# Optimization experiments

Measured on AMD Instinct MI355X. Metric: run time of the kernel, lower is better.

Reference implementation:

```python
import jax, jax.numpy as jnp
import numpy as np

EMBED_DIM = 1024
NUM_HEADS = 16
HEAD_DIM = EMBED_DIM // NUM_HEADS  # 64
SCALE = HEAD_DIM ** -0.5


def _rope_table(seq_len, dtype=jnp.float32):
    # inv_freq: [head_dim/2]
    inv_freq = 1.0 / (10000.0 ** (jnp.arange(0, HEAD_DIM, 2, dtype=dtype) / HEAD_DIM))
    t = jnp.arange(seq_len, dtype=dtype)
    freqs = t[:, None] * inv_freq[None, :]  # [S, hd/2]
    return jnp.sin(freqs), jnp.cos(freqs)


def _apply_rope(x, sin, cos):
    # x: [B, H, S, hd]; sin/cos: [S, hd/2]
    sin = sin[None, None]
    cos = cos[None, None]
    x_even = x[..., 0::2]
    x_odd = x[..., 1::2]
    new_even = x_even * cos - x_odd * sin
    new_odd = x_even * sin + x_odd * cos
    # interleave back: [..., hd/2, 2] -> [..., hd]
    return jnp.stack((new_even, new_odd), axis=-1).reshape(x.shape)


def setup_inputs() -> dict:
    key = jax.random.key(0)
    ks = jax.random.split(key, 9)
    B, S, D = 2, 2048, EMBED_DIM
    s = D ** -0.5
    return {
        "query": jax.random.normal(ks[0], (B, S, D), dtype=jnp.float32),
        "Wq": jax.random.normal(ks[1], (2 * D, D), dtype=jnp.float32) * s,
        "bq": jnp.zeros((2 * D,), dtype=jnp.float32),
        "Wk": jax.random.normal(ks[2], (D, D), dtype=jnp.float32) * s,
        "bk": jnp.zeros((D,), dtype=jnp.float32),
        "Wv": jax.random.normal(ks[3], (D, D), dtype=jnp.float32) * s,
        "bv": jnp.zeros((D,), dtype=jnp.float32),
        "Wo": jax.random.normal(ks[4], (D, D), dtype=jnp.float32) * s,
        "bo": jnp.zeros((D,), dtype=jnp.float32),
    }


def reference(query, Wq, bq, Wk, bk, Wv, bv, Wo, bo):
    B, S, D = query.shape
    H, hd = NUM_HEADS, HEAD_DIM

    # QKV projections (elementwise-gate variant: q_proj outputs 2*D)
    q_raw = (query @ Wq.T + bq).reshape(B, S, H, 2 * hd)
    q = q_raw[..., :hd].transpose(0, 2, 1, 3)          # [B,H,S,hd]
    gate = q_raw[..., hd:].transpose(0, 2, 1, 3)        # [B,H,S,hd]
    k = (query @ Wk.T + bk).reshape(B, S, H, hd).transpose(0, 2, 1, 3)
    v = (query @ Wv.T + bv).reshape(B, S, H, hd).transpose(0, 2, 1, 3)

    sin, cos = _rope_table(S)
    q = _apply_rope(q, sin, cos)
    k = _apply_rope(k, sin, cos)

    # scaled dot-product attention (no mask, non-causal, dropout=0)
    scores = jnp.einsum('bhqd,bhkd->bhqk', q, k) * SCALE
    probs = jax.nn.softmax(scores, axis=-1)
    attn = jnp.einsum('bhqk,bhkd->bhqd', probs, v)

    # sigmoid elementwise gate, then output projection
    attn = attn * jax.nn.sigmoid(gate)
    out = attn.transpose(0, 2, 1, 3).reshape(B, S, D)
    return out @ Wo.T + bo
```

## Files before the change

### kernel.cpp

```cpp
#include <hip/hip_runtime.h>
#include <math.h>

#define SEQ 2048
#define DIMD 1024
#define NH 16
#define HDIM 64

typedef _Float16 h8 __attribute__((ext_vector_type(8)));
typedef _Float16 h4 __attribute__((ext_vector_type(4)));
typedef __fp16 fp16x2 __attribute__((ext_vector_type(2)));
typedef float f32x4 __attribute__((ext_vector_type(4)));

__device__ __forceinline__ int SWE(int r, int c) {
  return ((r << 6) + c) ^ ((r & 7) << 3);
}

#define R0 16384
#define R1 (R0 + 1048576)
#define R2 (R1 + 524288)
#define R3 (R2 + 262144)
#define R4 (R3 + 262144)
#define R5 (R4 + 262144)

__global__ void prep_kernel(const float* __restrict__ query,
                            const float* __restrict__ Wq,
                            const float* __restrict__ Wk,
                            const float* __restrict__ Wv,
                            const float* __restrict__ Wo,
                            _Float16* __restrict__ Ah,
                            _Float16* __restrict__ Wqh,
                            _Float16* __restrict__ Wkh,
                            _Float16* __restrict__ Wvh,
                            _Float16* __restrict__ Woh,
                            _Float16* __restrict__ Wol,
                            float* __restrict__ sintab,
                            float* __restrict__ costab) {
  int i = blockIdx.x * 256 + threadIdx.x;
  if (i < R0) {
#pragma unroll
    for (int j = 0; j < 4; ++j) {
      int idx = i * 4 + j;
      int tp = idx >> 5;
      int fi = idx & 31;
      double inv = pow(10000.0, -(double)(2 * fi) / 64.0);
      double a = (double)tp * inv;
      sintab[idx] = (float)sin(a);
      costab[idx] = (float)cos(a);
    }
    return;
  }
  const float* src;
  _Float16* dst;
  int k;
  if (i < R1) {
    k = i - R0; src = query; dst = Ah;
  } else if (i < R2) {
    k = i - R1; src = Wq; dst = Wqh;
  } else if (i < R3) {
    k = i - R2; src = Wk; dst = Wkh;
  } else if (i < R4) {
    k = i - R3; src = Wv; dst = Wvh;
  } else if (i < R5) {
    k = i - R4;
    float4 v = ((const float4*)Wo)[k];
    h4 H, L;
    H[0] = (_Float16)v.x; L[0] = (_Float16)(v.x - (float)H[0]);
    H[1] = (_Float16)v.y; L[1] = (_Float16)(v.y - (float)H[1]);
    H[2] = (_Float16)v.z; L[2] = (_Float16)(v.z - (float)H[2]);
    H[3] = (_Float16)v.w; L[3] = (_Float16)(v.w - (float)H[3]);
    ((h4*)Woh)[k] = H;
    ((h4*)Wol)[k] = L;
    return;
  } else {
    return;
  }
  float4 v = ((const float4*)src)[k];
  h4 H;
  H[0] = (_Float16)v.x;
  H[1] = (_Float16)v.y;
  H[2] = (_Float16)v.z;
  H[3] = (_Float16)v.w;
  ((h4*)dst)[k] = H;
}

__global__ __launch_bounds__(256, 3) void qkv_kernel(
    const _Float16* __restrict__ Ah, const _Float16* __restrict__ Wqh,
    const _Float16* __restrict__ Wkh, const _Float16* __restrict__ Wvh,
    const float* __restrict__ bq, const float* __restrict__ bk,
    const float* __restrict__ bv, _Float16* __restrict__ qw,
    _Float16* __restrict__ sg, _Float16* __restrict__ kw,
    _Float16* __restrict__ vtw, const float* __restrict__ sintab,
    const float* __restrict__ costab) {
  __shared__ _Float16 Ash[8192];
  __shared__ _Float16 Bsh[8192];
  const int t = threadIdx.x;
  const int lane = t & 63;
  const int w = t >> 6;
  const int wm = w & 1, wn = w >> 1;
  const int fr = lane & 15;
  const int g = lane >> 4;
  const int m0 = blockIdx.y * 128;
  const int n0 = blockIdx.x * 128;
  const int region = (n0 < 2048) ? 0 : (n0 < 3072 ? 1 : 2);
  const _Float16* Wb = region == 0   ? Wqh + (size_t)n0 * DIMD
                       : region == 1 ? Wkh + (size_t)(n0 - 2048) * DIMD
                                     : Wvh + (size_t)(n0 - 3072) * DIMD;
  const float* bias = region == 0   ? bq + n0
                      : region == 1 ? bk + (n0 - 2048)
                                    : bv + (n0 - 3072);

  f32x4 acc[4][4];
#pragma unroll
  for (int i = 0; i < 4; ++i)
#pragma unroll
    for (int j = 0; j < 4; ++j) acc[i][j] = (f32x4){0.f, 0.f, 0.f, 0.f};

  const int srow = t >> 1;
  const int sc = (t & 1) * 32;
  const _Float16* pA = Ah + (size_t)(m0 + srow) * DIMD + sc;
  const _Float16* pW = Wb + (size_t)srow * DIMD + sc;

  h8 ra0 = *(const h8*)(pA);
  h8 ra1 = *(const h8*)(pA + 8);
  h8 ra2 = *(const h8*)(pA + 16);
  h8 ra3 = *(const h8*)(pA + 24);
  h8 rb0 = *(const h8*)(pW);
  h8 rb1 = *(const h8*)(pW + 8);
  h8 rb2 = *(const h8*)(pW + 16);
  h8 rb3 = *(const h8*)(pW + 24);

  for (int k0 = 0; k0 < DIMD; k0 += 64) {
    __syncthreads();
    *(h8*)&Ash[SWE(srow, sc + 0)] = ra0;
    *(h8*)&Ash[SWE(srow, sc + 8)] = ra1;
    *(h8*)&Ash[SWE(srow, sc + 16)] = ra2;
    *(h8*)&Ash[SWE(srow, sc + 24)] = ra3;
    *(h8*)&Bsh[SWE(srow, sc + 0)] = rb0;
    *(h8*)&Bsh[SWE(srow, sc + 8)] = rb1;
    *(h8*)&Bsh[SWE(srow, sc + 16)] = rb2;
    *(h8*)&Bsh[SWE(srow, sc + 24)] = rb3;
    __syncthreads();
    if (k0 + 64 < DIMD) {
      ra0 = *(const h8*)(pA + k0 + 64);
      ra1 = *(const h8*)(pA + k0 + 72);
      ra2 = *(const h8*)(pA + k0 + 80);
      ra3 = *(const h8*)(pA + k0 + 88);
      rb0 = *(const h8*)(pW + k0 + 64);
      rb1 = *(const h8*)(pW + k0 + 72);
      rb2 = *(const h8*)(pW + k0 + 80);
      rb3 = *(const h8*)(pW + k0 + 88);
    }
#pragma unroll
    for (int s = 0; s < 2; ++s) {
      h8 av[4], bv[4];
#pragma unroll
      for (int mi = 0; mi < 4; ++mi)
        av[mi] = *(const h8*)&Ash[SWE(wm * 64 + mi * 16 + fr, 8 * g + 32 * s)];
#pragma unroll
      for (int ni = 0; ni < 4; ++ni)
        bv[ni] = *(const h8*)&Bsh[SWE(wn * 64 + ni * 16 + fr, 8 * g + 32 * s)];
      __builtin_amdgcn_s_setprio(1);
#pragma unroll
      for (int mi = 0; mi < 4; ++mi)
#pragma unroll
        for (int ni = 0; ni < 4; ++ni)
          acc[mi][ni] = __builtin_amdgcn_mfma_f32_16x16x32_f16(
              av[mi], bv[ni], acc[mi][ni], 0, 0, 0);
      __builtin_amdgcn_s_setprio(0);
    }
  }

#pragma unroll
  for (int mi = 0; mi < 4; ++mi)
#pragma unroll
    for (int ni = 0; ni < 4; ++ni) {
      const int cl = wn * 64 + ni * 16 + fr;
      const float bsv = bias[cl];
#pragma unroll
      for (int r = 0; r < 4; ++r) {
        const int row = m0 + wm * 64 + mi * 16 + (lane >> 4) * 4 + r;
        float v = acc[mi][ni][r] + bsv;
        const int b = row >> 11;
        const int s = row & (SEQ - 1);
        if (region == 0) {
          const int h = n0 >> 7;
          const int d = cl & 63;
          if (wn == 0) {
            float vp = __shfl_xor(v, 1);
            const int pi = s * 32 + (d >> 1);
            float sn = sintab[pi], cs = costab[pi];
            float rv = (d & 1) ? (vp * sn + v * cs) : (v * cs - vp * sn);
            rv *= 0.125f;
            qw[((size_t)(b * NH + h) * SEQ + s) * HDIM + d] = (_Float16)rv;
          } else {
            float gv = 1.0f / (1.0f + __expf(-v));
            sg[((size_t)(b * SEQ + s)) * DIMD + h * HDIM + d] = (_Float16)gv;
          }
        } else if (region == 1) {
          const int kc = (n0 - 2048) + cl;
          const int h = kc >> 6, d = kc & 63;
          float vp = __shfl_xor(v, 1);
          const int pi = s * 32 + (d >> 1);
          float sn = sintab[pi], cs = costab[pi];
          float rv = (d & 1) ? (vp * sn + v * cs) : (v * cs - vp * sn);
          kw[((size_t)(b * NH + h) * SEQ + s) * HDIM + d] = (_Float16)rv;
        } else {
          const int vc = (n0 - 3072) + cl;
          const int h = vc >> 6, d = vc & 63;
          vtw[((size_t)(b * NH + h) * HDIM + d) * SEQ + s] = (_Float16)v;
        }
      }
    }
}

__global__ __launch_bounds__(256, 2) void ogemm_kernel(
    const _Float16* __restrict__ Ah, const _Float16* __restrict__ Al,
    const _Float16* __restrict__ Wh, const _Float16* __restrict__ Wl,
    const float* __restrict__ bias, float* __restrict__ out) {
  __shared__ _Float16 Ash[8192];
  __shared__ _Float16 Asl[8192];
  __shared__ _Float16 Bsh[4096];
  __shared__ _Float16 Bsl[4096];
  const int t = threadIdx.x;
  const int lane = t & 63;
  const int w = t >> 6;
  const int wm = w & 1, wn = w >> 1;
  const int fr = lane & 15;
  const int g = lane >> 4;
  const int m0 = blockIdx.y * 128, n0 = blockIdx.x * 64;

  f32x4 acc[4][2];
#pragma unroll
  for (int i = 0; i < 4; ++i)
#pragma unroll
    for (int j = 0; j < 2; ++j) acc[i][j] = (f32x4){0.f, 0.f, 0.f, 0.f};

  const int arow = t >> 1;
  const int ac = (t & 1) * 32;
  const int brow = t >> 2;
  const int bc = (t & 3) * 16;
  const _Float16* pAh = Ah + (size_t)(m0 + arow) * DIMD + ac;
  const _Float16* pAl = Al + (size_t)(m0 + arow) * DIMD + ac;
  const _Float16* pWh = Wh + (size_t)(n0 + brow) * DIMD + bc;
  const _Float16* pWl = Wl + (size_t)(n0 + brow) * DIMD + bc;

  h8 rah0 = *(const h8*)(pAh);
  h8 rah1 = *(const h8*)(pAh + 8);
  h8 rah2 = *(const h8*)(pAh + 16);
  h8 rah3 = *(const h8*)(pAh + 24);
  h8 ral0 = *(const h8*)(pAl);
  h8 ral1 = *(const h8*)(pAl + 8);
  h8 ral2 = *(const h8*)(pAl + 16);
  h8 ral3 = *(const h8*)(pAl + 24);
  h8 rbh0 = *(const h8*)(pWh);
  h8 rbh1 = *(const h8*)(pWh + 8);
  h8 rbl0 = *(const h8*)(pWl);
  h8 rbl1 = *(const h8*)(pWl + 8);

  for (int k0 = 0; k0 < DIMD; k0 += 64) {
    __syncthreads();
    *(h8*)&Ash[SWE(arow, ac + 0)] = rah0;
    *(h8*)&Ash[SWE(arow, ac + 8)] = rah1;
    *(h8*)&Ash[SWE(arow, ac + 16)] = rah2;
    *(h8*)&Ash[SWE(arow, ac + 24)] = rah3;
    *(h8*)&Asl[SWE(arow, ac + 0)] = ral0;
    *(h8*)&Asl[SWE(arow, ac + 8)] = ral1;
    *(h8*)&Asl[SWE(arow, ac + 16)] = ral2;
    *(h8*)&Asl[SWE(arow, ac + 24)] = ral3;
    *(h8*)&Bsh[SWE(brow, bc + 0)] = rbh0;
    *(h8*)&Bsh[SWE(brow, bc + 8)] = rbh1;
    *(h8*)&Bsl[SWE(brow, bc + 0)] = rbl0;
    *(h8*)&Bsl[SWE(brow, bc + 8)] = rbl1;
    __syncthreads();
    if (k0 + 64 < DIMD) {
      rah0 = *(const h8*)(pAh + k0 + 64);
      rah1 = *(const h8*)(pAh + k0 + 72);
      rah2 = *(const h8*)(pAh + k0 + 80);
      rah3 = *(const h8*)(pAh + k0 + 88);
      ral0 = *(const h8*)(pAl + k0 + 64);
      ral1 = *(const h8*)(pAl + k0 + 72);
      ral2 = *(const h8*)(pAl + k0 + 80);
      ral3 = *(const h8*)(pAl + k0 + 88);
      rbh0 = *(const h8*)(pWh + k0 + 64);
      rbh1 = *(const h8*)(pWh + k0 + 72);
      rbl0 = *(const h8*)(pWl + k0 + 64);
      rbl1 = *(const h8*)(pWl + k0 + 72);
    }
#pragma unroll
    for (int s = 0; s < 2; ++s) {
      h8 ahv[4], alv[4], bhv[2], blv[2];
#pragma unroll
      for (int mi = 0; mi < 4; ++mi) {
        ahv[mi] = *(const h8*)&Ash[SWE(wm * 64 + mi * 16 + fr, 8 * g + 32 * s)];
        alv[mi] = *(const h8*)&Asl[SWE(wm * 64 + mi * 16 + fr, 8 * g + 32 * s)];
      }
#pragma unroll
      for (int ni = 0; ni < 2; ++ni) {
        bhv[ni] = *(const h8*)&Bsh[SWE(wn * 32 + ni * 16 + fr, 8 * g + 32 * s)];
        blv[ni] = *(const h8*)&Bsl[SWE(wn * 32 + ni * 16 + fr, 8 * g + 32 * s)];
      }
      __builtin_amdgcn_s_setprio(1);
#pragma unroll
      for (int mi = 0; mi < 4; ++mi)
#pragma unroll
        for (int ni = 0; ni < 2; ++ni) {
          acc[mi][ni] = __builtin_amdgcn_mfma_f32_16x16x32_f16(
              ahv[mi], bhv[ni], acc[mi][ni], 0, 0, 0);
          acc[mi][ni] = __builtin_amdgcn_mfma_f32_16x16x32_f16(
              ahv[mi], blv[ni], acc[mi][ni], 0, 0, 0);
          acc[mi][ni] = __builtin_amdgcn_mfma_f32_16x16x32_f16(
              alv[mi], bhv[ni], acc[mi][ni], 0, 0, 0);
        }
      __builtin_amdgcn_s_setprio(0);
    }
  }

#pragma unroll
  for (int mi = 0; mi < 4; ++mi)
#pragma unroll
    for (int ni = 0; ni < 2; ++ni) {
      const int col = n0 + wn * 32 + ni * 16 + fr;
      const float bsv = bias[col];
#pragma unroll
      for (int r = 0; r < 4; ++r) {
        const int row = m0 + wm * 64 + mi * 16 + (lane >> 4) * 4 + r;
        out[(size_t)row * DIMD + col] = acc[mi][ni][r] + bsv;
      }
    }
}

__global__ __launch_bounds__(256) void flash_kernel(
    const _Float16* __restrict__ qh, const _Float16* __restrict__ kh,
    const _Float16* __restrict__ vt, const _Float16* __restrict__ sg,
    _Float16* __restrict__ agh, _Float16* __restrict__ agl) {
  __shared__ _Float16 K_lds[4096];
  __shared__ _Float16 Vt_lds[4096];
  const int t = threadIdx.x;
  const int lane = t & 63;
  const int w = t >> 6;
  const int fr = lane & 15;
  const int g = lane >> 4;
  const int bh = blockIdx.y;
  const int q0 = blockIdx.x * 64;
  const size_t kvbase = (size_t)bh * (SEQ * HDIM);

  h8 qb[2];
  {
    const _Float16* qp =
        qh + kvbase + (size_t)(q0 + 16 * w + fr) * HDIM + 8 * g;
    qb[0] = *(const h8*)(qp);
    qb[1] = *(const h8*)(qp + 32);
  }

  f32x4 oacc[4];
  float m_i = -1e30f, l_i = 0.f;
#pragma unroll
  for (int df = 0; df < 4; ++df) oacc[df] = (f32x4){0.f, 0.f, 0.f, 0.f};

  const int srow = t >> 2;
  const int scb = (t & 3) * 16;
  const _Float16* kp = kh + kvbase;
  const _Float16* vp = vt + kvbase + (size_t)srow * SEQ;

  for (int j0 = 0; j0 < SEQ; j0 += 64) {
    h8 k0v = *(const h8*)(kp + (size_t)(j0 + srow) * HDIM + scb);
    h8 k1v = *(const h8*)(kp + (size_t)(j0 + srow) * HDIM + scb + 8);
    h8 v0v = *(const h8*)(vp + j0 + scb);
    h8 v1v = *(const h8*)(vp + j0 + scb + 8);
    __syncthreads();
    *(h8*)&K_lds[SWE(srow, scb)] = k0v;
    *(h8*)&K_lds[SWE(srow, scb + 8)] = k1v;
    *(h8*)&Vt_lds[SWE(srow, scb)] = v0v;
    *(h8*)&Vt_lds[SWE(srow, scb + 8)] = v1v;
    __syncthreads();

    f32x4 sacc[4];
#pragma unroll
    for (int nf = 0; nf < 4; ++nf) sacc[nf] = (f32x4){0.f, 0.f, 0.f, 0.f};

    __builtin_amdgcn_s_setprio(1);
#pragma unroll
    for (int nf = 0; nf < 4; ++nf) {
      h8 ka0 = *(const h8*)&K_lds[SWE(16 * nf + fr, 8 * g)];
      h8 ka1 = *(const h8*)&K_lds[SWE(16 * nf + fr, 32 + 8 * g)];
      sacc[nf] =
          __builtin_amdgcn_mfma_f32_16x16x32_f16(ka0, qb[0], sacc[nf], 0, 0, 0);
      sacc[nf] =
          __builtin_amdgcn_mfma_f32_16x16x32_f16(ka1, qb[1], sacc[nf], 0, 0, 0);
    }
    __builtin_amdgcn_s_setprio(0);

    float m0 = fmaxf(fmaxf(sacc[0][0], sacc[0][1]), sacc[0][2]);
    float m1 = fmaxf(fmaxf(sacc[0][3], sacc[1][0]), sacc[1][1]);
    float m2 = fmaxf(fmaxf(sacc[1][2], sacc[1][3]), sacc[2][0]);
    float m3 = fmaxf(fmaxf(sacc[2][1], sacc[2][2]), sacc[2][3]);
    float m4 = fmaxf(fmaxf(sacc[3][0], sacc[3][1]), sacc[3][2]);
    float mx =
        fmaxf(fmaxf(fmaxf(fmaxf(m0, m1), m2), fmaxf(m3, m4)), sacc[3][3]);
    mx = fmaxf(mx, __shfl_xor(mx, 16));
    mx = fmaxf(mx, __shfl_xor(mx, 32));
    const int allskip = __all(mx <= m_i + 8.0f);
    const float mn = allskip ? m_i : fmaxf(m_i, mx);
    float p[4][4];
    float rs = 0.f;
#pragma unroll
    for (int nf = 0; nf < 4; ++nf)
#pragma unroll
      for (int r = 0; r < 4; ++r) {
        p[nf][r] = __expf(sacc[nf][r] - mn);
        rs += p[nf][r];
      }
    rs += __shfl_xor(rs, 16);
    rs += __shfl_xor(rs, 32);
    if (allskip) {
      l_i += rs;
    } else {
      float f = __expf(m_i - mn);
      l_i = l_i * f + rs;
      m_i = mn;
      f32x4 fv = (f32x4){f, f, f, f};
#pragma unroll
      for (int df = 0; df < 4; ++df) oacc[df] *= fv;
    }
    h8 pb[2];
#pragma unroll
    for (int m2 = 0; m2 < 2; ++m2) {
      union {
        h8 v;
        fp16x2 h[4];
      } u;
      u.h[0] = __builtin_amdgcn_cvt_pkrtz(p[2 * m2][0], p[2 * m2][1]);
      u.h[1] = __builtin_amdgcn_cvt_pkrtz(p[2 * m2][2], p[2 * m2][3]);
      u.h[2] = __builtin_amdgcn_cvt_pkrtz(p[2 * m2 + 1][0], p[2 * m2 + 1][1]);
      u.h[3] = __builtin_amdgcn_cvt_pkrtz(p[2 * m2 + 1][2], p[2 * m2 + 1][3]);
      pb[m2] = u.v;
    }

    __builtin_amdgcn_s_setprio(1);
#pragma unroll
    for (int df = 0; df < 4; ++df) {
#pragma unroll
      for (int m2 = 0; m2 < 2; ++m2) {
        h4 vlo = *(const h4*)&Vt_lds[SWE(16 * df + fr, 32 * m2 + 4 * g)];
        h4 vhi = *(const h4*)&Vt_lds[SWE(16 * df + fr, 32 * m2 + 16 + 4 * g)];
        h8 va;
#pragma unroll
        for (int r = 0; r < 4; ++r) {
          va[r] = vlo[r];
          va[4 + r] = vhi[r];
        }
        oacc[df] =
            __builtin_amdgcn_mfma_f32_16x16x32_f16(va, pb[m2], oacc[df], 0, 0, 0);
      }
    }
    __builtin_amdgcn_s_setprio(0);
  }

  const int b = bh >> 4, h = bh & 15;
  const int qrow = q0 + 16 * w + fr;
  const float inv = 1.0f / l_i;
  const size_t obase = ((size_t)(b * SEQ + qrow)) * DIMD + h * HDIM;
#pragma unroll
  for (int df = 0; df < 4; ++df) {
    const int d0 = 16 * df + 4 * g;
    h4 gt = *(const h4*)&sg[obase + d0];
    h4 HI, LO;
#pragma unroll
    for (int r = 0; r < 4; ++r) {
      float val = oacc[df][r] * inv * (float)gt[r];
      _Float16 hi = (_Float16)val;
      HI[r] = hi;
      LO[r] = (_Float16)(val - (float)hi);
    }
    *(h4*)&agh[obase + d0] = HI;
    *(h4*)&agl[obase + d0] = LO;
  }
}

extern "C" void kernel_launch(void* const* d_in, const int* in_sizes, int n_in,
                              void* d_out, int out_size, void* d_ws,
                              size_t ws_size, hipStream_t stream) {
  const float* query = (const float*)d_in[0];
  const float* Wq = (const float*)d_in[1];
  const float* bq = (const float*)d_in[2];
  const float* Wk = (const float*)d_in[3];
  const float* bk = (const float*)d_in[4];
  const float* Wv = (const float*)d_in[5];
  const float* bv = (const float*)d_in[6];
  const float* Wo = (const float*)d_in[7];
  const float* bo = (const float*)d_in[8];
  float* out = (float*)d_out;

  float* fws = (float*)d_ws;
  float* sintab = fws;
  float* costab = fws + 65536;
  _Float16* Ah = (_Float16*)(fws + 131072);
  _Float16* Al = Ah + 4194304;
  _Float16* Wqh = Al + 4194304;
  _Float16* Wkh = Wqh + 2097152;
  _Float16* Wvh = Wkh + 1048576;
  _Float16* Woh = Wvh + 1048576;
  _Float16* Wol = Woh + 1048576;
  _Float16* qw = Wol + 1048576;
  _Float16* kw = qw + 4194304;
  _Float16* vtw = kw + 4194304;
  _Float16* sg = vtw + 4194304;
  _Float16* agh = Ah;
  _Float16* agl = Al;

  prep_kernel<<<9280, 256, 0, stream>>>(query, Wq, Wk, Wv, Wo, Ah, Wqh, Wkh,
                                        Wvh, Woh, Wol, sintab, costab);

  qkv_kernel<<<dim3(32, 32), 256, 0, stream>>>(Ah, Wqh, Wkh, Wvh, bq, bk, bv,
                                               qw, sg, kw, vtw, sintab, costab);

  flash_kernel<<<dim3(32, 32), 256, 0, stream>>>(qw, kw, vtw, sg, agh, agl);

  ogemm_kernel<<<dim3(16, 32), 256, 0, stream>>>(agh, agl, Woh, Wol, bo, out);
}
```

Measured before the change: 178.6 us.

## Use async global-to-LDS double buffering, XCD-swizzled grids, and single-fp16 output GEMM

The QKV and output GEMMs now stage tiles with global_load_lds into double-buffered LDS, which overlaps the next tile's load with the current MFMA work. All three main kernels map a 1D grid through an XCD-aware block swizzle to improve L2 locality. The output projection drops the split hi/lo fp16 compensation, cutting its MFMA count to a third and removing the low-part buffers. The flash kernel prefetches the next K/V tile into registers, and the V-transpose store is vectorized. The single-fp16 output GEMM lowers accuracy, which may matter against the tolerance.

```diff
diff --git a/kernel.cpp b/kernel.cpp
--- a/kernel.cpp
+++ b/kernel.cpp
@@ -10,6 +10,9 @@
 typedef _Float16 h4 __attribute__((ext_vector_type(4)));
 typedef __fp16 fp16x2 __attribute__((ext_vector_type(2)));
 typedef float f32x4 __attribute__((ext_vector_type(4)));
+
+typedef const __attribute__((address_space(1))) void* gas_t;
+typedef __attribute__((address_space(3))) void* las_t;
 
 __device__ __forceinline__ int SWE(int r, int c) {
   return ((r << 6) + c) ^ ((r & 7) << 3);
@@ -32,7 +35,6 @@
                             _Float16* __restrict__ Wkh,
                             _Float16* __restrict__ Wvh,
                             _Float16* __restrict__ Woh,
-                            _Float16* __restrict__ Wol,
                             float* __restrict__ sintab,
                             float* __restrict__ costab) {
   int i = blockIdx.x * 256 + threadIdx.x;
@@ -61,16 +63,7 @@
   } else if (i < R4) {
     k = i - R3; src = Wv; dst = Wvh;
   } else if (i < R5) {
-    k = i - R4;
-    float4 v = ((const float4*)Wo)[k];
-    h4 H, L;
-    H[0] = (_Float16)v.x; L[0] = (_Float16)(v.x - (float)H[0]);
-    H[1] = (_Float16)v.y; L[1] = (_Float16)(v.y - (float)H[1]);
-    H[2] = (_Float16)v.z; L[2] = (_Float16)(v.z - (float)H[2]);
-    H[3] = (_Float16)v.w; L[3] = (_Float16)(v.w - (float)H[3]);
-    ((h4*)Woh)[k] = H;
-    ((h4*)Wol)[k] = L;
-    return;
+    k = i - R4; src = Wo; dst = Woh;
   } else {
     return;
   }
@@ -83,7 +76,7 @@
   ((h4*)dst)[k] = H;
 }
 
-__global__ __launch_bounds__(256, 3) void qkv_kernel(
+__global__ __launch_bounds__(256) void qkv_kernel(
     const _Float16* __restrict__ Ah, const _Float16* __restrict__ Wqh,
     const _Float16* __restrict__ Wkh, const _Float16* __restrict__ Wvh,
     const float* __restrict__ bq, const float* __restrict__ bk,
@@ -91,16 +84,18 @@
     _Float16* __restrict__ sg, _Float16* __restrict__ kw,
     _Float16* __restrict__ vtw, const float* __restrict__ sintab,
     const float* __restrict__ costab) {
-  __shared__ _Float16 Ash[8192];
-  __shared__ _Float16 Bsh[8192];
+  __shared__ _Float16 Abuf[2][8192];
+  __shared__ _Float16 Bbuf[2][8192];
   const int t = threadIdx.x;
   const int lane = t & 63;
   const int w = t >> 6;
   const int wm = w & 1, wn = w >> 1;
   const int fr = lane & 15;
   const int g = lane >> 4;
-  const int m0 = blockIdx.y * 128;
-  const int n0 = blockIdx.x * 128;
+  const int flat = blockIdx.x;
+  const int swz = (flat & 7) * 128 + (flat >> 3);
+  const int m0 = (swz >> 5) * 128;
+  const int n0 = (swz & 31) * 128;
   const int region = (n0 < 2048) ? 0 : (n0 < 3072 ? 1 : 2);
   const _Float16* Wb = region == 0   ? Wqh + (size_t)n0 * DIMD
                        : region == 1 ? Wkh + (size_t)(n0 - 2048) * DIMD
@@ -115,50 +110,44 @@
 #pragma unroll
     for (int j = 0; j < 4; ++j) acc[i][j] = (f32x4){0.f, 0.f, 0.f, 0.f};
 
-  const int srow = t >> 1;
-  const int sc = (t & 1) * 32;
-  const _Float16* pA = Ah + (size_t)(m0 + srow) * DIMD + sc;
-  const _Float16* pW = Wb + (size_t)srow * DIMD + sc;
-
-  h8 ra0 = *(const h8*)(pA);
-  h8 ra1 = *(const h8*)(pA + 8);
-  h8 ra2 = *(const h8*)(pA + 16);
-  h8 ra3 = *(const h8*)(pA + 24);
-  h8 rb0 = *(const h8*)(pW);
-  h8 rb1 = *(const h8*)(pW + 8);
-  h8 rb2 = *(const h8*)(pW + 16);
-  h8 rb3 = *(const h8*)(pW + 24);
-
-  for (int k0 = 0; k0 < DIMD; k0 += 64) {
-    __syncthreads();
-    *(h8*)&Ash[SWE(srow, sc + 0)] = ra0;
-    *(h8*)&Ash[SWE(srow, sc + 8)] = ra1;
-    *(h8*)&Ash[SWE(srow, sc + 16)] = ra2;
-    *(h8*)&Ash[SWE(srow, sc + 24)] = ra3;
-    *(h8*)&Bsh[SWE(srow, sc + 0)] = rb0;
-    *(h8*)&Bsh[SWE(srow, sc + 8)] = rb1;
-    *(h8*)&Bsh[SWE(srow, sc + 16)] = rb2;
-    *(h8*)&Bsh[SWE(srow, sc + 24)] = rb3;
-    __syncthreads();
-    if (k0 + 64 < DIMD) {
-      ra0 = *(const h8*)(pA + k0 + 64);
-      ra1 = *(const h8*)(pA + k0 + 72);
-      ra2 = *(const h8*)(pA + k0 + 80);
-      ra3 = *(const h8*)(pA + k0 + 88);
-      rb0 = *(const h8*)(pW + k0 + 64);
-      rb1 = *(const h8*)(pW + k0 + 72);
-      rb2 = *(const h8*)(pW + k0 + 80);
-      rb3 = *(const h8*)(pW + k0 + 88);
-    }
+  const int rsub = lane >> 3;
+  const int csw = ((lane & 7) ^ rsub) << 3;
+  const _Float16* gA = Ah + (size_t)(m0 + w * 32 + rsub) * DIMD + csw;
+  const _Float16* gB = Wb + (size_t)(w * 32 + rsub) * DIMD + csw;
+  const int ldsb = w * 2048;
+
+  auto stage = [&](int kt, int pb) {
+#pragma unroll
+    for (int i = 0; i < 4; ++i) {
+      __builtin_amdgcn_global_load_lds(
+          (gas_t)(gA + (size_t)i * 8 * DIMD + kt * 64),
+          (las_t)&Abuf[pb][ldsb + i * 512], 16, 0, 0);
+      __builtin_amdgcn_global_load_lds(
+          (gas_t)(gB + (size_t)i * 8 * DIMD + kt * 64),
+          (las_t)&Bbuf[pb][ldsb + i * 512], 16, 0, 0);
+    }
+  };
+
+  stage(0, 0);
+  for (int kt = 0; kt < 16; ++kt) {
+    const int pb = kt & 1;
+    if (kt < 15) {
+      stage(kt + 1, pb ^ 1);
+      asm volatile("s_waitcnt vmcnt(8)" ::: "memory");
+    } else {
+      asm volatile("s_waitcnt vmcnt(0)" ::: "memory");
+    }
+    __builtin_amdgcn_sched_barrier(0);
+    __builtin_amdgcn_s_barrier();
 #pragma unroll
     for (int s = 0; s < 2; ++s) {
       h8 av[4], bv[4];
 #pragma unroll
       for (int mi = 0; mi < 4; ++mi)
-        av[mi] = *(const h8*)&Ash[SWE(wm * 64 + mi * 16 + fr, 8 * g + 32 * s)];
+        av[mi] = *(const h8*)&Abuf[pb][SWE(wm * 64 + mi * 16 + fr, 8 * g + 32 * s)];
 #pragma unroll
       for (int ni = 0; ni < 4; ++ni)
-        bv[ni] = *(const h8*)&Bsh[SWE(wn * 64 + ni * 16 + fr, 8 * g + 32 * s)];
+        bv[ni] = *(const h8*)&Bbuf[pb][SWE(wn * 64 + ni * 16 + fr, 8 * g + 32 * s)];
       __builtin_amdgcn_s_setprio(1);
 #pragma unroll
       for (int mi = 0; mi < 4; ++mi)
@@ -168,6 +157,7 @@
               av[mi], bv[ni], acc[mi][ni], 0, 0, 0);
       __builtin_amdgcn_s_setprio(0);
     }
+    __builtin_amdgcn_s_barrier();
   }
 
 #pragma unroll
@@ -176,9 +166,21 @@
     for (int ni = 0; ni < 4; ++ni) {
       const int cl = wn * 64 + ni * 16 + fr;
       const float bsv = bias[cl];
+      if (region == 2) {
+        const int vc = (n0 - 3072) + cl;
+        const int h = vc >> 6, d = vc & 63;
+        const int row0 = m0 + wm * 64 + mi * 16 + g * 4;
+        const int b = row0 >> 11;
+        const int s0 = row0 & (SEQ - 1);
+        h4 vv;
+#pragma unroll
+        for (int r = 0; r < 4; ++r) vv[r] = (_Float16)(acc[mi][ni][r] + bsv);
+        *(h4*)&vtw[((size_t)(b * NH + h) * HDIM + d) * SEQ + s0] = vv;
+        continue;
+      }
 #pragma unroll
       for (int r = 0; r < 4; ++r) {
-        const int row = m0 + wm * 64 + mi * 16 + (lane >> 4) * 4 + r;
+        const int row = m0 + wm * 64 + mi * 16 + g * 4 + r;
         float v = acc[mi][ni][r] + bsv;
         const int b = row >> 11;
         const int s = row & (SEQ - 1);
@@ -196,7 +198,7 @@
             float gv = 1.0f / (1.0f + __expf(-v));
             sg[((size_t)(b * SEQ + s)) * DIMD + h * HDIM + d] = (_Float16)gv;
           }
-        } else if (region == 1) {
+        } else {
           const int kc = (n0 - 2048) + cl;
           const int h = kc >> 6, d = kc & 63;
           float vp = __shfl_xor(v, 1);
@@ -204,30 +206,26 @@
           float sn = sintab[pi], cs = costab[pi];
           float rv = (d & 1) ? (vp * sn + v * cs) : (v * cs - vp * sn);
           kw[((size_t)(b * NH + h) * SEQ + s) * HDIM + d] = (_Float16)rv;
-        } else {
-          const int vc = (n0 - 3072) + cl;
-          const int h = vc >> 6, d = vc & 63;
-          vtw[((size_t)(b * NH + h) * HDIM + d) * SEQ + s] = (_Float16)v;
         }
       }
     }
 }
 
-__global__ __launch_bounds__(256, 2) void ogemm_kernel(
-    const _Float16* __restrict__ Ah, const _Float16* __restrict__ Al,
-    const _Float16* __restrict__ Wh, const _Float16* __restrict__ Wl,
+__global__ __launch_bounds__(256) void ogemm_kernel(
+    const _Float16* __restrict__ ag, const _Float16* __restrict__ Woh,
     const float* __restrict__ bias, float* __restrict__ out) {
-  __shared__ _Float16 Ash[8192];
-  __shared__ _Float16 Asl[8192];
-  __shared__ _Float16 Bsh[4096];
-  __shared__ _Float16 Bsl[4096];
+  __shared__ _Float16 Abuf[2][8192];
+  __shared__ _Float16 Bbuf[2][4096];
   const int t = threadIdx.x;
   const int lane = t & 63;
   const int w = t >> 6;
   const int wm = w & 1, wn = w >> 1;
   const int fr = lane & 15;
   const int g = lane >> 4;
-  const int m0 = blockIdx.y * 128, n0 = blockIdx.x * 64;
+  const int flat = blockIdx.x;
+  const int swz = (flat & 7) * 64 + (flat >> 3);
+  const int m0 = (swz >> 4) * 128;
+  const int n0 = (swz & 15) * 64;
 
   f32x4 acc[4][2];
 #pragma unroll
@@ -235,84 +233,56 @@
 #pragma unroll
     for (int j = 0; j < 2; ++j) acc[i][j] = (f32x4){0.f, 0.f, 0.f, 0.f};
 
-  const int arow = t >> 1;
-  const int ac = (t & 1) * 32;
-  const int brow = t >> 2;
-  const int bc = (t & 3) * 16;
-  const _Float16* pAh = Ah + (size_t)(m0 + arow) * DIMD + ac;
-  const _Float16* pAl = Al + (size_t)(m0 + arow) * DIMD + ac;
-  const _Float16* pWh = Wh + (size_t)(n0 + brow) * DIMD + bc;
-  const _Float16* pWl = Wl + (size_t)(n0 + brow) * DIMD + bc;
-
-  h8 rah0 = *(const h8*)(pAh);
-  h8 rah1 = *(const h8*)(pAh + 8);
-  h8 rah2 = *(const h8*)(pAh + 16);
-  h8 rah3 = *(const h8*)(pAh + 24);
-  h8 ral0 = *(const h8*)(pAl);
-  h8 ral1 = *(const h8*)(pAl + 8);
-  h8 ral2 = *(const h8*)(pAl + 16);
-  h8 ral3 = *(const h8*)(pAl + 24);
-  h8 rbh0 = *(const h8*)(pWh);
-  h8 rbh1 = *(const h8*)(pWh + 8);
-  h8 rbl0 = *(const h8*)(pWl);
-  h8 rbl1 = *(const h8*)(pWl + 8);
-
-  for (int k0 = 0; k0 < DIMD; k0 += 64) {
-    __syncthreads();
-    *(h8*)&Ash[SWE(arow, ac + 0)] = rah0;
-    *(h8*)&Ash[SWE(arow, ac + 8)] = rah1;
-    *(h8*)&Ash[SWE(arow, ac + 16)] = rah2;
-    *(h8*)&Ash[SWE(arow, ac + 24)] = rah3;
-    *(h8*)&Asl[SWE(arow, ac + 0)] = ral0;
-    *(h8*)&Asl[SWE(arow, ac + 8)] = ral1;
-    *(h8*)&Asl[SWE(arow, ac + 16)] = ral2;
-    *(h8*)&Asl[SWE(arow, ac + 24)] = ral3;
-    *(h8*)&Bsh[SWE(brow, bc + 0)] = rbh0;
-    *(h8*)&Bsh[SWE(brow, bc + 8)] = rbh1;
-    *(h8*)&Bsl[SWE(brow, bc + 0)] = rbl0;
-    *(h8*)&Bsl[SWE(brow, bc + 8)] = rbl1;
-    __syncthreads();
-    if (k0 + 64 < DIMD) {
-      rah0 = *(const h8*)(pAh + k0 + 64);
-      rah1 = *(const h8*)(pAh + k0 + 72);
-      rah2 = *(const h8*)(pAh + k0 + 80);
-      rah3 = *(const h8*)(pAh + k0 + 88);
-      ral0 = *(const h8*)(pAl + k0 + 64);
-      ral1 = *(const h8*)(pAl + k0 + 72);
-      ral2 = *(const h8*)(pAl + k0 + 80);
-      ral3 = *(const h8*)(pAl + k0 + 88);
-      rbh0 = *(const h8*)(pWh + k0 + 64);
-      rbh1 = *(const h8*)(pWh + k0 + 72);
-      rbl0 = *(const h8*)(pWl + k0 + 64);
-      rbl1 = *(const h8*)(pWl + k0 + 72);
-    }
+  const int rsub = lane >> 3;
+  const int csw = ((lane & 7) ^ rsub) << 3;
+  const _Float16* gA = ag + (size_t)(m0 + w * 32 + rsub) * DIMD + csw;
+  const _Float16* gB = Woh + (size_t)(n0 + w * 16 + rsub) * DIMD + csw;
+  const int ldsbA = w * 2048;
+  const int ldsbB = w * 1024;
+
+  auto stage = [&](int kt, int pb) {
+#pragma unroll
+    for (int i = 0; i < 4; ++i)
+      __builtin_amdgcn_global_load_lds(
+          (gas_t)(gA + (size_t)i * 8 * DIMD + kt * 64),
+          (las_t)&Abuf[pb][ldsbA + i * 512], 16, 0, 0);
+#pragma unroll
+    for (int i = 0; i < 2; ++i)
+      __builtin_amdgcn_global_load_lds(
+          (gas_t)(gB + (size_t)i * 8 * DIMD + kt * 64),
+          (las_t)&Bbuf[pb][ldsbB + i * 512], 16, 0, 0);
+  };
+
+  stage(0, 0);
+  for (int kt = 0; kt < 16; ++kt) {
+    const int pb = kt & 1;
+    if (kt < 15) {
+      stage(kt + 1, pb ^ 1);
+      asm volatile("s_waitcnt vmcnt(6)" ::: "memory");
+    } else {
+      asm volatile("s_waitcnt vmcnt(0)" ::: "memory");
+    }
+    __builtin_amdgcn_sched_barrier(0);
+    __builtin_amdgcn_s_barrier();
 #pragma unroll
     for (int s = 0; s < 2; ++s) {
-      h8 ahv[4], alv[4], bhv[2], blv[2];
-#pragma unroll
-      for (int mi = 0; mi < 4; ++mi) {
-        ahv[mi] = *(const h8*)&Ash[SWE(wm * 64 + mi * 16 + fr, 8 * g + 32 * s)];
-        alv[mi] = *(const h8*)&Asl[SWE(wm * 64 + mi * 16 + fr, 8 * g + 32 * s)];
-      }
-#pragma unroll
-      for (int ni = 0; ni < 2; ++ni) {
-        bhv[ni] = *(const h8*)&Bsh[SWE(wn * 32 + ni * 16 + fr, 8 * g + 32 * s)];
-        blv[ni] = *(const h8*)&Bsl[SWE(wn * 32 + ni * 16 + fr, 8 * g + 32 * s)];
-      }
+      h8 av[4], bv[2];
+#pragma unroll
+      for (int mi = 0; mi < 4; ++mi)
+        av[mi] = *(const h8*)&Abuf[pb][SWE(wm * 64 + mi * 16 + fr, 8 * g + 32 * s)];
+#pragma unroll
+      for (int ni = 0; ni < 2; ++ni)
+        bv[ni] = *(const h8*)&Bbuf[pb][SWE(wn * 32 + ni * 16 + fr, 8 * g + 32 * s)];
       __builtin_amdgcn_s_setprio(1);
 #pragma unroll
       for (int mi = 0; mi < 4; ++mi)
 #pragma unroll
-        for (int ni = 0; ni < 2; ++ni) {
+        for (int ni = 0; ni < 2; ++ni)
           acc[mi][ni] = __builtin_amdgcn_mfma_f32_16x16x32_f16(
-              ahv[mi], bhv[ni], acc[mi][ni], 0, 0, 0);
-          acc[mi][ni] = __builtin_amdgcn_mfma_f32_16x16x32_f16(
-              ahv[mi], blv[ni], acc[mi][ni], 0, 0, 0);
-          acc[mi][ni] = __builtin_amdgcn_mfma_f32_16x16x32_f16(
-              alv[mi], bhv[ni], acc[mi][ni], 0, 0, 0);
-        }
+              av[mi], bv[ni], acc[mi][ni], 0, 0, 0);
       __builtin_amdgcn_s_setprio(0);
     }
+    __builtin_amdgcn_s_barrier();
   }
 
 #pragma unroll
@@ -323,7 +293,7 @@
       const float bsv = bias[col];
 #pragma unroll
       for (int r = 0; r < 4; ++r) {
-        const int row = m0 + wm * 64 + mi * 16 + (lane >> 4) * 4 + r;
+        const int row = m0 + wm * 64 + mi * 16 + g * 4 + r;
         out[(size_t)row * DIMD + col] = acc[mi][ni][r] + bsv;
       }
     }
@@ -332,7 +302,7 @@
 __global__ __launch_bounds__(256) void flash_kernel(
     const _Float16* __restrict__ qh, const _Float16* __restrict__ kh,
     const _Float16* __restrict__ vt, const _Float16* __restrict__ sg,
-    _Float16* __restrict__ agh, _Float16* __restrict__ agl) {
+    _Float16* __restrict__ ag) {
   __shared__ _Float16 K_lds[4096];
   __shared__ _Float16 Vt_lds[4096];
   const int t = threadIdx.x;
@@ -340,14 +310,15 @@
   const int w = t >> 6;
   const int fr = lane & 15;
   const int g = lane >> 4;
-  const int bh = blockIdx.y;
-  const int q0 = blockIdx.x * 64;
+  const int flat = blockIdx.x;
+  const int swz = (flat & 7) * 128 + (flat >> 3);
+  const int bh = swz >> 5;
+  const int q0 = (swz & 31) * 64;
   const size_t kvbase = (size_t)bh * (SEQ * HDIM);
 
   h8 qb[2];
   {
-    const _Float16* qp =
-        qh + kvbase + (size_t)(q0 + 16 * w + fr) * HDIM + 8 * g;
+    const _Float16* qp = qh + kvbase + (size_t)(q0 + 16 * w + fr) * HDIM + 8 * g;
     qb[0] = *(const h8*)(qp);
     qb[1] = *(const h8*)(qp + 32);
   }
@@ -362,16 +333,23 @@
   const _Float16* kp = kh + kvbase;
   const _Float16* vp = vt + kvbase + (size_t)srow * SEQ;
 
+  h8 k0v = *(const h8*)(kp + (size_t)srow * HDIM + scb);
+  h8 k1v = *(const h8*)(kp + (size_t)srow * HDIM + scb + 8);
+  h8 v0v = *(const h8*)(vp + scb);
+  h8 v1v = *(const h8*)(vp + scb + 8);
+
   for (int j0 = 0; j0 < SEQ; j0 += 64) {
-    h8 k0v = *(const h8*)(kp + (size_t)(j0 + srow) * HDIM + scb);
-    h8 k1v = *(const h8*)(kp + (size_t)(j0 + srow) * HDIM + scb + 8);
-    h8 v0v = *(const h8*)(vp + j0 + scb);
-    h8 v1v = *(const h8*)(vp + j0 + scb + 8);
     __syncthreads();
     *(h8*)&K_lds[SWE(srow, scb)] = k0v;
     *(h8*)&K_lds[SWE(srow, scb + 8)] = k1v;
     *(h8*)&Vt_lds[SWE(srow, scb)] = v0v;
     *(h8*)&Vt_lds[SWE(srow, scb + 8)] = v1v;
+    if (j0 + 64 < SEQ) {
+      k0v = *(const h8*)(kp + (size_t)(j0 + 64 + srow) * HDIM + scb);
+      k1v = *(const h8*)(kp + (size_t)(j0 + 64 + srow) * HDIM + scb + 8);
+      v0v = *(const h8*)(vp + j0 + 64 + scb);
+      v1v = *(const h8*)(vp + j0 + 64 + scb + 8);
+    }
     __syncthreads();
 
     f32x4 sacc[4];
@@ -424,25 +402,25 @@
     }
     h8 pb[2];
 #pragma unroll
-    for (int m2 = 0; m2 < 2; ++m2) {
+    for (int m2i = 0; m2i < 2; ++m2i) {
       union {
         h8 v;
         fp16x2 h[4];
       } u;
-      u.h[0] = __builtin_amdgcn_cvt_pkrtz(p[2 * m2][0], p[2 * m2][1]);
-      u.h[1] = __builtin_amdgcn_cvt_pkrtz(p[2 * m2][2], p[2 * m2][3]);
-      u.h[2] = __builtin_amdgcn_cvt_pkrtz(p[2 * m2 + 1][0], p[2 * m2 + 1][1]);
-      u.h[3] = __builtin_amdgcn_cvt_pkrtz(p[2 * m2 + 1][2], p[2 * m2 + 1][3]);
-      pb[m2] = u.v;
+      u.h[0] = __builtin_amdgcn_cvt_pkrtz(p[2 * m2i][0], p[2 * m2i][1]);
+      u.h[1] = __builtin_amdgcn_cvt_pkrtz(p[2 * m2i][2], p[2 * m2i][3]);
+      u.h[2] = __builtin_amdgcn_cvt_pkrtz(p[2 * m2i + 1][0], p[2 * m2i + 1][1]);
+      u.h[3] = __builtin_amdgcn_cvt_pkrtz(p[2 * m2i + 1][2], p[2 * m2i + 1][3]);
+      pb[m2i] = u.v;
     }
 
     __builtin_amdgcn_s_setprio(1);
 #pragma unroll
     for (int df = 0; df < 4; ++df) {
 #pragma unroll
-      for (int m2 = 0; m2 < 2; ++m2) {
-        h4 vlo = *(const h4*)&Vt_lds[SWE(16 * df + fr, 32 * m2 + 4 * g)];
-        h4 vhi = *(const h4*)&Vt_lds[SWE(16 * df + fr, 32 * m2 + 16 + 4 * g)];
+      for (int m2i = 0; m2i < 2; ++m2i) {
+        h4 vlo = *(const h4*)&Vt_lds[SWE(16 * df + fr, 32 * m2i + 4 * g)];
+        h4 vhi = *(const h4*)&Vt_lds[SWE(16 * df + fr, 32 * m2i + 16 + 4 * g)];
         h8 va;
 #pragma unroll
         for (int r = 0; r < 4; ++r) {
@@ -450,7 +428,7 @@
           va[4 + r] = vhi[r];
         }
         oacc[df] =
-            __builtin_amdgcn_mfma_f32_16x16x32_f16(va, pb[m2], oacc[df], 0, 0, 0);
+            __builtin_amdgcn_mfma_f32_16x16x32_f16(va, pb[m2i], oacc[df], 0, 0, 0);
       }
     }
     __builtin_amdgcn_s_setprio(0);
@@ -464,16 +442,11 @@
   for (int df = 0; df < 4; ++df) {
     const int d0 = 16 * df + 4 * g;
     h4 gt = *(const h4*)&sg[obase + d0];
-    h4 HI, LO;
-#pragma unroll
-    for (int r = 0; r < 4; ++r) {
-      float val = oacc[df][r] * inv * (float)gt[r];
-      _Float16 hi = (_Float16)val;
-      HI[r] = hi;
-      LO[r] = (_Float16)(val - (float)hi);
-    }
-    *(h4*)&agh[obase + d0] = HI;
-    *(h4*)&agl[obase + d0] = LO;
+    h4 ov;
+#pragma unroll
+    for (int r = 0; r < 4; ++r)
+      ov[r] = (_Float16)(oacc[df][r] * inv * (float)gt[r]);
+    *(h4*)&ag[obase + d0] = ov;
   }
 }
 
@@ -495,26 +468,23 @@
   float* sintab = fws;
   float* costab = fws + 65536;
   _Float16* Ah = (_Float16*)(fws + 131072);
-  _Float16* Al = Ah + 4194304;
-  _Float16* Wqh = Al + 4194304;
+  _Float16* Wqh = Ah + 4194304;
   _Float16* Wkh = Wqh + 2097152;
   _Float16* Wvh = Wkh + 1048576;
   _Float16* Woh = Wvh + 1048576;
-  _Float16* Wol = Woh + 1048576;
-  _Float16* qw = Wol + 1048576;
+  _Float16* qw = Woh + 1048576;
   _Float16* kw = qw + 4194304;
   _Float16* vtw = kw + 4194304;
   _Float16* sg = vtw + 4194304;
-  _Float16* agh = Ah;
-  _Float16* agl = Al;
+  _Float16* ag = Ah;
 
   prep_kernel<<<9280, 256, 0, stream>>>(query, Wq, Wk, Wv, Wo, Ah, Wqh, Wkh,
-                                        Wvh, Woh, Wol, sintab, costab);
-
-  qkv_kernel<<<dim3(32, 32), 256, 0, stream>>>(Ah, Wqh, Wkh, Wvh, bq, bk, bv,
-                                               qw, sg, kw, vtw, sintab, costab);
-
-  flash_kernel<<<dim3(32, 32), 256, 0, stream>>>(qw, kw, vtw, sg, agh, agl);
-
-  ogemm_kernel<<<dim3(16, 32), 256, 0, stream>>>(agh, agl, Woh, Wol, bo, out);
-}
+                                        Wvh, Woh, sintab, costab);
+
+  qkv_kernel<<<1024, 256, 0, stream>>>(Ah, Wqh, Wkh, Wvh, bq, bk, bv, qw, sg,
+                                       kw, vtw, sintab, costab);
+
+  flash_kernel<<<1024, 256, 0, stream>>>(qw, kw, vtw, sg, ag);
+
+  ogemm_kernel<<<512, 256, 0, stream>>>(ag, Woh, bo, out);
+}
```

Measured after the change: 157.2 us. 1.14x faster.
